# Performance work log

Measured on AMD Instinct MI355X. Metric: run time of the kernel, lower is better.

## Reference

```python
import jax, jax.numpy as jnp
jax.config.update("jax_enable_x64", True)
import numpy as np

VOXEL_SIZE = 0.1   # size_scheduler.value
VBITS = 12         # bits per voxel coordinate (signed, offset by VOFF)
VMASK = (1 << VBITS) - 1
VOFF = 1 << (VBITS - 1)
GBITS = 10         # bits for group index (G=1024)


def setup_inputs() -> dict:
    key = jax.random.key(0)
    B, G, P, F = 64, 1024, 64, 3
    active_pred = jax.random.normal(key, (B * G, P, F), dtype=jnp.float32)
    active_mask = jnp.ones((B, G), dtype=bool)  # all active -> static nonzero count
    return {"active_pred": active_pred, "active_mask": active_mask}


def reference(active_pred, active_mask):
    N, P, F = active_pred.shape
    # active_mask.nonzero() -> [N, 2] (batch, group) ids
    bi, gi = jnp.nonzero(active_mask, size=N)
    bg = jnp.stack([bi, gi], axis=1).astype(jnp.int64)              # [N, 2]
    bg = jnp.broadcast_to(bg[:, None, :], (N, P, 2)).reshape(-1, 2)  # [N*P, 2]
    offsets = active_pred.reshape(-1, F)[:, :3]                      # [N*P, 3]
    vox = jnp.floor(offsets / VOXEL_SIZE).astype(jnp.int64)          # [N*P, 3]
    # Pack (b, g, vx, vy, vz) into one int64 key; packing is lexicographic-order
    # preserving, so sorted-unique of codes == torch.unique(dim=0) row order.
    v = vox + VOFF                                                   # nonnegative
    code = ((((bg[:, 0] << GBITS) | bg[:, 1]) << (3 * VBITS))
            | (v[:, 0] << (2 * VBITS)) | (v[:, 1] << VBITS) | v[:, 2])
    ucode, cluster_indices = jnp.unique(
        code, return_inverse=True, size=code.shape[0], fill_value=jnp.max(code))
    # Decode unique codes back to [U, 5] keys (padded tail repeats max key).
    ub = ucode >> (3 * VBITS + GBITS)
    ug = (ucode >> (3 * VBITS)) & ((1 << GBITS) - 1)
    uv0 = ((ucode >> (2 * VBITS)) & VMASK) - VOFF
    uv1 = ((ucode >> VBITS) & VMASK) - VOFF
    uv2 = (ucode & VMASK) - VOFF
    unique_keys = jnp.stack([ub, ug, uv0, uv1, uv2], axis=1)
    return unique_keys, cluster_indices
```

## Files before the change

kernel.cpp:

```cpp
#include <hip/hip_runtime.h>
#include <cstdint>

typedef unsigned long long u64;
typedef unsigned int u32;
typedef int i4 __attribute__((ext_vector_type(4), aligned(4)));

constexpr int VBITS = 12;
constexpr int VOFF  = 1 << (VBITS - 1);
constexpr int GBITS = 10;

constexpr int GPB = 16;
constexpr int WPB = 4;
constexpr int GPW = 4;

__device__ inline u32 partner_xor(u32 k, int j) {
    switch (j) {
    case 1:  return (u32)__builtin_amdgcn_mov_dpp((int)k, 0xB1, 0xF, 0xF, true);
    case 2:  return (u32)__builtin_amdgcn_mov_dpp((int)k, 0x4E, 0xF, 0xF, true);
    case 4:  return (u32)__builtin_amdgcn_ds_swizzle((int)k, 0x101F);
    case 8:  return (u32)__builtin_amdgcn_ds_swizzle((int)k, 0x201F);
    case 16: return (u32)__builtin_amdgcn_ds_swizzle((int)k, 0x401F);
    default: return (u32)__shfl_xor((int)k, 32, 64);
    }
}

__device__ inline u32 wave_sort_u32(u32 k, int lane) {
    #pragma unroll
    for (int ks = 2; ks <= 64; ks <<= 1) {
        #pragma unroll
        for (int j = ks >> 1; j >= 1; j >>= 1) {
            u32 other = partner_xor(k, j);
            bool takeMin = ((lane & ks) == 0) == ((lane & j) == 0);
            u32 mn = min(k, other), mx = max(k, other);
            k = takeMin ? mn : mx;
        }
    }
    return k;
}

__device__ inline void wave_sort_u32x2(u32& k0, u32& k1, int lane) {
    #pragma unroll
    for (int ks = 2; ks <= 64; ks <<= 1) {
        #pragma unroll
        for (int j = ks >> 1; j >= 1; j >>= 1) {
            u32 o0 = partner_xor(k0, j);
            u32 o1 = partner_xor(k1, j);
            bool takeMin = ((lane & ks) == 0) == ((lane & j) == 0);
            u32 mn0 = min(k0, o0), mx0 = max(k0, o0);
            u32 mn1 = min(k1, o1), mx1 = max(k1, o1);
            k0 = takeMin ? mn0 : mx0;
            k1 = takeMin ? mn1 : mx1;
        }
    }
}

__device__ inline u64 wave_sort_u64(u64 k, int lane) {
    #pragma unroll
    for (int ks = 2; ks <= 64; ks <<= 1) {
        #pragma unroll
        for (int j = ks >> 1; j >= 1; j >>= 1) {
            u64 other = __shfl_xor(k, j, 64);
            bool takeMin = ((lane & ks) == 0) == ((lane & j) == 0);
            u64 mn = k < other ? k : other;
            u64 mx = k < other ? other : k;
            k = takeMin ? mn : mx;
        }
    }
    return k;
}

__device__ inline u32 lane_push(int dest_lane, u32 src) {
    return (u32)__builtin_amdgcn_ds_permute(dest_lane << 2, (int)src);
}

__device__ inline u32 post_sort_pack(u32 k, int lane, int r0, int r1, int r2,
                                     int gid, u32* __restrict__ arr,
                                     u64* __restrict__ meta) {
    u32 sk = k >> 6;
    u32 pv = __shfl_up(sk, 1, 64);
    int flag = (lane == 0 || sk != pv) ? 1 : 0;
    u64 bal = __ballot(flag);
    int rank = (int)__popcll(bal & ((1ull << lane) - 1ull)) + flag - 1;
    u32 cnt = (u32)__popcll(bal);
    int orig = (int)(k & 63);

    u32 dByRank = lane_push(rank, sk);
    u32 rByOrig = lane_push(orig, (u32)rank);
    u32 packed = (dByRank & 0xFFFFFFu) | (rByOrig << 24);

    if (lane == 0)
        meta[gid] = ((u64)((u32)(r0 - 128) & 4095))
                  | ((u64)((u32)(r1 - 128) & 4095) << 12)
                  | ((u64)((u32)(r2 - 128) & 4095) << 24)
                  | ((u64)cnt << 48);
    arr[(size_t)gid * 64 + lane] = packed;
    return cnt;
}

__device__ inline u32 process_group_single(const float* __restrict__ q, int lane,
                                           int gid, u32* __restrict__ arr,
                                           u64* __restrict__ meta) {
    int v0 = (int)floorf(q[0] / 0.1f) + VOFF;
    int v1 = (int)floorf(q[1] / 0.1f) + VOFF;
    int v2 = (int)floorf(q[2] / 0.1f) + VOFF;
    int r0 = __shfl(v0, 0, 64), r1 = __shfl(v1, 0, 64), r2 = __shfl(v2, 0, 64);
    int d0 = v0 - r0 + 128, d1 = v1 - r1 + 128, d2 = v2 - r2 + 128;
    bool bad = ((u32)(d0 | d1 | d2) > 255u) || ((u32)(v0 | v1 | v2) > 4095u);

    if (!__any(bad)) {
        u32 k = ((u32)d0 << 22) | ((u32)d1 << 14) | ((u32)d2 << 6) | (u32)lane;
        k = wave_sort_u32(k, lane);
        return post_sort_pack(k, lane, r0, r1, r2, gid, arr, meta);
    } else {
        u64 code = ((u64)(long long)v0 << 24) | ((u64)(long long)v1 << 12)
                 | (u64)(long long)v2;
        u64 k = wave_sort_u64((code << 6) | (u64)lane, lane);
        u64 sk = k >> 6, pv = __shfl_up(sk, 1, 64);
        int flag = (lane == 0 || sk != pv) ? 1 : 0;
        u64 bal = __ballot(flag);
        int rank = (int)__popcll(bal & ((1ull << lane) - 1ull)) + flag - 1;
        u32 cnt = (u32)__popcll(bal);
        int orig = (int)(k & 63);
        u32 rByOrig = lane_push(orig, (u32)rank);
        if (lane == 0) meta[gid] = ((u64)cnt << 48) | (1ull << 56);
        arr[(size_t)gid * 64 + lane] = rByOrig << 24;
        return cnt;
    }
}

__global__ __launch_bounds__(256) void vox_build(
    const float* __restrict__ pred,
    u32* __restrict__ arr,
    u64* __restrict__ meta,
    u32* __restrict__ blockSums,
    int ngroups)
{
    __shared__ u32 s_ws[WPB];
    const int t = threadIdx.x, w = t >> 6, lane = t & 63, b = blockIdx.x;

    u32 wsum = 0;
    for (int jp = 0; jp < GPW; jp += 2) {
        int gid0 = b * GPB + w * GPW + jp, gid1 = gid0 + 1;

        if (gid1 < ngroups) {
            const float* q0 = pred + (size_t)gid0 * 192 + lane * 3;
            const float* q1 = q0 + 192;

            int a0 = (int)floorf(q0[0] / 0.1f) + VOFF;
            int a1 = (int)floorf(q0[1] / 0.1f) + VOFF;
            int a2 = (int)floorf(q0[2] / 0.1f) + VOFF;
            int c0 = (int)floorf(q1[0] / 0.1f) + VOFF;
            int c1 = (int)floorf(q1[1] / 0.1f) + VOFF;
            int c2 = (int)floorf(q1[2] / 0.1f) + VOFF;

            int ra0 = __shfl(a0, 0, 64), ra1 = __shfl(a1, 0, 64), ra2 = __shfl(a2, 0, 64);
            int rc0 = __shfl(c0, 0, 64), rc1 = __shfl(c1, 0, 64), rc2 = __shfl(c2, 0, 64);
            int da0 = a0 - ra0 + 128, da1 = a1 - ra1 + 128, da2 = a2 - ra2 + 128;
            int dc0 = c0 - rc0 + 128, dc1 = c1 - rc1 + 128, dc2 = c2 - rc2 + 128;
            bool bad0 = ((u32)(da0 | da1 | da2) > 255u) || ((u32)(a0 | a1 | a2) > 4095u);
            bool bad1 = ((u32)(dc0 | dc1 | dc2) > 255u) || ((u32)(c0 | c1 | c2) > 4095u);

            if (!__any(bad0 || bad1)) {
                u32 k0 = ((u32)da0 << 22) | ((u32)da1 << 14) | ((u32)da2 << 6) | (u32)lane;
                u32 k1 = ((u32)dc0 << 22) | ((u32)dc1 << 14) | ((u32)dc2 << 6) | (u32)lane;
                wave_sort_u32x2(k0, k1, lane);
                wsum += post_sort_pack(k0, lane, ra0, ra1, ra2, gid0, arr, meta);
                wsum += post_sort_pack(k1, lane, rc0, rc1, rc2, gid1, arr, meta);
            } else {
                wsum += process_group_single(q0, lane, gid0, arr, meta);
                wsum += process_group_single(q1, lane, gid1, arr, meta);
            }
        } else if (gid0 < ngroups) {
            const float* q0 = pred + (size_t)gid0 * 192 + lane * 3;
            wsum += process_group_single(q0, lane, gid0, arr, meta);
        }
    }
    if (lane == 0) s_ws[w] = wsum;
    __syncthreads();
    if (t == 0) blockSums[b] = s_ws[0] + s_ws[1] + s_ws[2] + s_ws[3];
}

__global__ __launch_bounds__(256) void vox_emit(
    const float* __restrict__ pred,
    const u32* __restrict__ arr,
    const u64* __restrict__ meta,
    const u32* __restrict__ blockSums,
    int* __restrict__ okeys,
    int* __restrict__ inv,
    int ngroups, int totalrows, int nblocks)
{
    __shared__ u32 s_scr[512];
    __shared__ int s_row[WPB][336];
    __shared__ u32 s_c[GPB];
    __shared__ u32 s_baseU[2];
    __shared__ int s_tail[5];
    const int t = threadIdx.x, w = t >> 6, lane = t & 63, b = blockIdx.x;

    u32 a[GPW]; u64 m[GPW];
    #pragma unroll
    for (int j = 0; j < GPW; ++j) {
        int gid = b * GPB + w * GPW + j;
        if (gid < ngroups) {
            a[j] = arr[(size_t)gid * 64 + lane];
            m[j] = meta[gid];
        } else { a[j] = 0; m[j] = 0; }
    }

    if (t < GPB) {
        int gid = b * GPB + t;
        s_c[t] = (gid < ngroups) ? (u32)((meta[gid] >> 48) & 127) : 0;
    }

    {
        u32 below = 0, all = 0;
        for (int i = t; i < nblocks; i += 256) {
            u32 v = blockSums[i];
            all += v;
            if (i < b) below += v;
        }
        __syncthreads();
        s_scr[t] = below; s_scr[256 + t] = all;
        __syncthreads();
        #pragma unroll
        for (int off = 128; off >= 1; off >>= 1) {
            if (t < off) {
                s_scr[t]       += s_scr[t + off];
                s_scr[256 + t] += s_scr[256 + t + off];
            }
            __syncthreads();
        }
        if (t == 0) { s_baseU[0] = s_scr[0]; s_baseU[1] = s_scr[256]; }
        __syncthreads();
    }

    u32 base = s_baseU[0];
    #pragma unroll
    for (int i = 0; i < GPB; i++) if (i < w * GPW) base += s_c[i];

    int* buf = s_row[w];

    #pragma unroll
    for (int j = 0; j < GPW; ++j) {
        int gid = b * GPB + w * GPW + j;
        if (gid < ngroups) {
            u32 cnt = (u32)((m[j] >> 48) & 127);
            u32 rinv = a[j] >> 24;

            inv[(size_t)gid * 64 + lane] = (int)(base + rinv);

            const int bb = gid >> GBITS;
            const int gg = gid & ((1 << GBITS) - 1);
            int* dst = okeys + (size_t)base * 5;

            if (!((m[j] >> 56) & 1)) {
                u32 m0 = (u32)m[j] & 4095, m1 = (u32)(m[j] >> 12) & 4095,
                    m2 = (u32)(m[j] >> 24) & 4095;
                u32 d = a[j] & 0xFFFFFFu;
                if ((u32)lane < cnt) {
                    int* row = buf + lane * 5;
                    row[0] = bb;
                    row[1] = gg;
                    row[2] = (int)((m0 + ((d >> 16) & 255u)) & 4095u) - VOFF;
                    row[3] = (int)((m1 + ((d >> 8) & 255u)) & 4095u) - VOFF;
                    row[4] = (int)((m2 + (d & 255u)) & 4095u) - VOFF;
                }
                asm volatile("" ::: "memory");

                u32 n5 = cnt * 5u, n5r = n5 & ~3u;
                u32 p0 = 4u * (u32)lane;
                if (p0 < n5r) *(i4*)(dst + p0) = *(const i4*)(buf + p0);
                u32 p1 = 256u + 4u * (u32)lane;
                if (p1 < n5r) *(i4*)(dst + p1) = *(const i4*)(buf + p1);
                u32 rem = n5 - n5r;
                if ((u32)lane < rem) dst[n5r + lane] = buf[n5r + lane];
            } else {
                const float* p = pred + (size_t)gid * 192 + lane * 3;
                long long w0 = (long long)floorf(p[0] / 0.1f) + VOFF;
                long long w1 = (long long)floorf(p[1] / 0.1f) + VOFF;
                long long w2 = (long long)floorf(p[2] / 0.1f) + VOFF;
                u64 code = ((u64)w0 << 24) | ((u64)w1 << 12) | (u64)w2;
                u32 clo = lane_push((int)rinv, (u32)code);
                u32 chi = lane_push((int)rinv, (u32)(code >> 32));
                u64 c = ((u64)chi << 32) | clo;
                if (lane < (int)cnt) {
                    int* row = dst + (size_t)lane * 5;
                    row[0] = bb; row[1] = gg;
                    row[2] = (int)((c >> 24) & 4095) - VOFF;
                    row[3] = (int)((c >> 12) & 4095) - VOFF;
                    row[4] = (int)(c & 4095) - VOFF;
                }
            }
            base += cnt;
        }
    }

    if (w == 0) {
        int lg = ngroups - 1;
        const float* p = pred + (size_t)lg * 192 + lane * 3;
        long long w0 = (long long)floorf(p[0] / 0.1f) + VOFF;
        long long w1 = (long long)floorf(p[1] / 0.1f) + VOFF;
        long long w2 = (long long)floorf(p[2] / 0.1f) + VOFF;
        u64 code = ((u64)w0 << 24) | ((u64)w1 << 12) | (u64)w2;
        #pragma unroll
        for (int off = 32; off >= 1; off >>= 1) {
            u64 o = __shfl_xor(code, off, 64);
            code = (o > code) ? o : code;
        }
        if (lane == 0) {
            s_tail[0] = lg >> GBITS;
            s_tail[1] = lg & ((1 << GBITS) - 1);
            s_tail[2] = (int)((code >> 24) & 4095) - VOFF;
            s_tail[3] = (int)((code >> 12) & 4095) - VOFF;
            s_tail[4] = (int)(code & 4095) - VOFF;
        }
    }
    __syncthreads();
    {
        u32 U = s_baseU[1];
        u32 total5 = (u32)totalrows * 5u;
        u32 stride = (u32)gridDim.x * 256u;
        for (u32 e = U * 5u + (u32)b * 256u + (u32)t; e < total5; e += stride)
            okeys[e] = s_tail[e % 5u];
    }
}

extern "C" void kernel_launch(void* const* d_in, const int* in_sizes, int n_in,
                              void* d_out, int out_size, void* d_ws, size_t ws_size,
                              hipStream_t stream)
{
    const float* pred = (const float*)d_in[0];
    int ngroups   = in_sizes[1];
    int totalrows = in_sizes[0] / 3;
    int nblocks   = (ngroups + GPB - 1) / GPB;

    int* okeys = (int*)d_out;
    int* inv   = okeys + (size_t)totalrows * 5;

    char* ws = (char*)d_ws;
    u64* meta      = (u64*)ws;
    u32* arr       = (u32*)(meta + ngroups);
    u32* blockSums = arr + (size_t)ngroups * 64;

    vox_build<<<nblocks, 256, 0, stream>>>(pred, arr, meta, blockSums, ngroups);
    vox_emit<<<nblocks, 256, 0, stream>>>(pred, arr, meta, blockSums,
                                          okeys, inv, ngroups, totalrows, nblocks);
}
```

Baseline: 48.47 us.

## Process 64 groups per emit block with shared-memory wave scan of offsets

The emit kernel now handles 64 groups per block instead of 16, with each wave covering 16 groups in chunks of 4. Group metadata is staged in shared memory and per-group output offsets come from a wave-level prefix scan rather than a serial accumulation. This cuts the number of blocks, and with it the redundant blockSums reduction each block performs over all previous blocks, since nblocks shrinks fourfold. The cost is fewer blocks in flight and more serial work per wave.

```diff
diff --git a/kernel.cpp b/kernel.cpp
--- a/kernel.cpp
+++ b/kernel.cpp
@@ -9,9 +9,9 @@
 constexpr int VOFF  = 1 << (VBITS - 1);
 constexpr int GBITS = 10;
 
-constexpr int GPB = 16;
+constexpr int GPB = 64;
 constexpr int WPB = 4;
-constexpr int GPW = 4;
+constexpr int GPW = 16;
 
 __device__ inline u32 partner_xor(u32 k, int j) {
     switch (j) {
@@ -192,23 +192,17 @@
     __shared__ u32 s_scr[512];
     __shared__ int s_row[WPB][336];
     __shared__ u32 s_c[GPB];
+    __shared__ u32 s_off[GPB];
+    __shared__ u64 s_m[GPB];
     __shared__ u32 s_baseU[2];
     __shared__ int s_tail[5];
     const int t = threadIdx.x, w = t >> 6, lane = t & 63, b = blockIdx.x;
 
-    u32 a[GPW]; u64 m[GPW];
-    #pragma unroll
-    for (int j = 0; j < GPW; ++j) {
-        int gid = b * GPB + w * GPW + j;
-        if (gid < ngroups) {
-            a[j] = arr[(size_t)gid * 64 + lane];
-            m[j] = meta[gid];
-        } else { a[j] = 0; m[j] = 0; }
-    }
-
     if (t < GPB) {
         int gid = b * GPB + t;
-        s_c[t] = (gid < ngroups) ? (u32)((meta[gid] >> 48) & 127) : 0;
+        u64 mm = (gid < ngroups) ? meta[gid] : 0;
+        s_m[t] = mm;
+        s_c[t] = (u32)((mm >> 48) & 127);
     }
 
     {
@@ -233,64 +227,87 @@
         __syncthreads();
     }
 
-    u32 base = s_baseU[0];
-    #pragma unroll
-    for (int i = 0; i < GPB; i++) if (i < w * GPW) base += s_c[i];
-
+    if (w == 0) {
+        u32 x = s_c[lane];
+        u32 incl = x;
+        #pragma unroll
+        for (int off = 1; off < 64; off <<= 1) {
+            u32 v = __shfl_up(incl, off, 64);
+            if (lane >= off) incl += v;
+        }
+        s_off[lane] = incl - x;
+    }
+    __syncthreads();
+
+    const u32 blockBase = s_baseU[0];
     int* buf = s_row[w];
 
-    #pragma unroll
-    for (int j = 0; j < GPW; ++j) {
-        int gid = b * GPB + w * GPW + j;
-        if (gid < ngroups) {
-            u32 cnt = (u32)((m[j] >> 48) & 127);
-            u32 rinv = a[j] >> 24;
-
-            inv[(size_t)gid * 64 + lane] = (int)(base + rinv);
-
-            const int bb = gid >> GBITS;
-            const int gg = gid & ((1 << GBITS) - 1);
-            int* dst = okeys + (size_t)base * 5;
-
-            if (!((m[j] >> 56) & 1)) {
-                u32 m0 = (u32)m[j] & 4095, m1 = (u32)(m[j] >> 12) & 4095,
-                    m2 = (u32)(m[j] >> 24) & 4095;
-                u32 d = a[j] & 0xFFFFFFu;
-                if ((u32)lane < cnt) {
-                    int* row = buf + lane * 5;
-                    row[0] = bb;
-                    row[1] = gg;
-                    row[2] = (int)((m0 + ((d >> 16) & 255u)) & 4095u) - VOFF;
-                    row[3] = (int)((m1 + ((d >> 8) & 255u)) & 4095u) - VOFF;
-                    row[4] = (int)((m2 + (d & 255u)) & 4095u) - VOFF;
-                }
-                asm volatile("" ::: "memory");
-
-                u32 n5 = cnt * 5u, n5r = n5 & ~3u;
-                u32 p0 = 4u * (u32)lane;
-                if (p0 < n5r) *(i4*)(dst + p0) = *(const i4*)(buf + p0);
-                u32 p1 = 256u + 4u * (u32)lane;
-                if (p1 < n5r) *(i4*)(dst + p1) = *(const i4*)(buf + p1);
-                u32 rem = n5 - n5r;
-                if ((u32)lane < rem) dst[n5r + lane] = buf[n5r + lane];
-            } else {
-                const float* p = pred + (size_t)gid * 192 + lane * 3;
-                long long w0 = (long long)floorf(p[0] / 0.1f) + VOFF;
-                long long w1 = (long long)floorf(p[1] / 0.1f) + VOFF;
-                long long w2 = (long long)floorf(p[2] / 0.1f) + VOFF;
-                u64 code = ((u64)w0 << 24) | ((u64)w1 << 12) | (u64)w2;
-                u32 clo = lane_push((int)rinv, (u32)code);
-                u32 chi = lane_push((int)rinv, (u32)(code >> 32));
-                u64 c = ((u64)chi << 32) | clo;
-                if (lane < (int)cnt) {
-                    int* row = dst + (size_t)lane * 5;
-                    row[0] = bb; row[1] = gg;
-                    row[2] = (int)((c >> 24) & 4095) - VOFF;
-                    row[3] = (int)((c >> 12) & 4095) - VOFF;
-                    row[4] = (int)(c & 4095) - VOFF;
+    for (int c = 0; c < GPW; c += 4) {
+        u32 a[4]; u64 m[4];
+        #pragma unroll
+        for (int j = 0; j < 4; ++j) {
+            int idx = w * GPW + c + j;
+            int gid = b * GPB + idx;
+            if (gid < ngroups) {
+                a[j] = arr[(size_t)gid * 64 + lane];
+                m[j] = s_m[idx];
+            } else { a[j] = 0; m[j] = 0; }
+        }
+
+        #pragma unroll
+        for (int j = 0; j < 4; ++j) {
+            int idx = w * GPW + c + j;
+            int gid = b * GPB + idx;
+            if (gid < ngroups) {
+                u32 cnt = (u32)((m[j] >> 48) & 127);
+                u32 rinv = a[j] >> 24;
+                u32 base = blockBase + s_off[idx];
+
+                inv[(size_t)gid * 64 + lane] = (int)(base + rinv);
+
+                const int bb = gid >> GBITS;
+                const int gg = gid & ((1 << GBITS) - 1);
+                int* dst = okeys + (size_t)base * 5;
+
+                if (!((m[j] >> 56) & 1)) {
+                    u32 m0 = (u32)m[j] & 4095, m1 = (u32)(m[j] >> 12) & 4095,
+                        m2 = (u32)(m[j] >> 24) & 4095;
+                    u32 d = a[j] & 0xFFFFFFu;
+                    if ((u32)lane < cnt) {
+                        int* row = buf + lane * 5;
+                        row[0] = bb;
+                        row[1] = gg;
+                        row[2] = (int)((m0 + ((d >> 16) & 255u)) & 4095u) - VOFF;
+                        row[3] = (int)((m1 + ((d >> 8) & 255u)) & 4095u) - VOFF;
+                        row[4] = (int)((m2 + (d & 255u)) & 4095u) - VOFF;
+                    }
+                    asm volatile("" ::: "memory");
+
+                    u32 n5 = cnt * 5u, n5r = n5 & ~3u;
+                    u32 p0 = 4u * (u32)lane;
+                    if (p0 < n5r) *(i4*)(dst + p0) = *(const i4*)(buf + p0);
+                    u32 p1 = 256u + 4u * (u32)lane;
+                    if (p1 < n5r) *(i4*)(dst + p1) = *(const i4*)(buf + p1);
+                    u32 rem = n5 - n5r;
+                    if ((u32)lane < rem) dst[n5r + lane] = buf[n5r + lane];
+                } else {
+                    const float* p = pred + (size_t)gid * 192 + lane * 3;
+                    long long w0 = (long long)floorf(p[0] / 0.1f) + VOFF;
+                    long long w1 = (long long)floorf(p[1] / 0.1f) + VOFF;
+                    long long w2 = (long long)floorf(p[2] / 0.1f) + VOFF;
+                    u64 code = ((u64)w0 << 24) | ((u64)w1 << 12) | (u64)w2;
+                    u32 clo = lane_push((int)rinv, (u32)code);
+                    u32 chi = lane_push((int)rinv, (u32)(code >> 32));
+                    u64 cc = ((u64)chi << 32) | clo;
+                    if (lane < (int)cnt) {
+                        int* row = dst + (size_t)lane * 5;
+                        row[0] = bb; row[1] = gg;
+                        row[2] = (int)((cc >> 24) & 4095) - VOFF;
+                        row[3] = (int)((cc >> 12) & 4095) - VOFF;
+                        row[4] = (int)(cc & 4095) - VOFF;
+                    }
                 }
             }
-            base += cnt;
         }
     }
 
```

New measurement: 49.57 us. +2.3%, slower.
